# Performance work log

Hardware: AMD Instinct MI355X
Metric: run time of the kernel (lower is better)

Reference implementation:

```python
import jax, jax.numpy as jnp
import numpy as np

V, N, K, D = 100000, 20000, 32, 128
NEG = -1e9  # masked logit value


def setup_inputs() -> dict:
    key = jax.random.key(0)
    ks = jax.random.split(key, 8)
    return {
        "nodes": jax.random.randint(ks[0], (N,), 0, V),
        "neigh_idx": jax.random.randint(ks[1], (N, K), 0, V),
        "degrees": jax.random.randint(ks[2], (N,), 0, K + 1),
        "u2e": jax.random.normal(ks[3], (V, D), dtype=jnp.float32),
        "W1": jax.random.normal(ks[4], (2 * D, D), dtype=jnp.float32) * 0.05,
        "b1": jnp.zeros((D,), jnp.float32),
        "W2": jax.random.normal(ks[5], (D, D), dtype=jnp.float32) * 0.05,
        "b2": jnp.zeros((D,), jnp.float32),
        "W3": jax.random.normal(ks[6], (D, 1), dtype=jnp.float32) * 0.05,
        "b3": jnp.zeros((1,), jnp.float32),
    }


def reference(nodes, neigh_idx, degrees, u2e, W1, b1, W2, b2, W3, b3):
    self_feats = u2e[nodes]                      # [N, D]
    e_u = u2e[neigh_idx]                         # [N, K, D] ragged gather (padded)
    # Attention MLP: cat(neighbor, self) -> relu -> relu -> scalar logit
    x = jnp.concatenate([e_u, jnp.broadcast_to(self_feats[:, None, :], (e_u.shape[0], K, D))], axis=-1)  # [N, K, 2D]
    h = jax.nn.relu(x @ W1 + b1)                 # [N, K, D]
    h = jax.nn.relu(h @ W2 + b2)                 # [N, K, D]
    logits = (h @ W3 + b3)[..., 0]               # [N, K]
    mask = jnp.arange(K)[None, :] < degrees[:, None]
    att = jax.nn.softmax(jnp.where(mask, logits, NEG), axis=-1)  # softmax over neighbors
    agg = jnp.einsum("nk,nkd->nd", att, e_u)     # attention-weighted neighbor sum
    out = jnp.where(degrees[:, None] > 0, (agg + self_feats) * 0.5, self_feats)
    return out
```

## Files before the change

### kernel.cpp

```cpp
#include <hip/hip_runtime.h>
#include <hip/hip_bf16.h>

#define KK 32
#define DD 128
#define NEGV (-1e9f)
#define SE 136

typedef __attribute__((ext_vector_type(8))) short bf16x8;
typedef __attribute__((ext_vector_type(4))) float f32x4;

__device__ __forceinline__ unsigned short f2bf(float f) {
    union { float f; unsigned u; } v; v.f = f;
    unsigned r = v.u + 0x7fffu + ((v.u >> 16) & 1u);
    return (unsigned short)(r >> 16);
}
__device__ __forceinline__ float bf2f(unsigned short h) {
    union { unsigned u; float f; } v; v.u = ((unsigned)h) << 16;
    return v.f;
}
__device__ __forceinline__ unsigned pk2(float x, float y) {
    union { __hip_bfloat162 h; unsigned u; } c;
    c.h = __float22bfloat162_rn(float2{x, y});
    return c.u;
}

__global__ __launch_bounds__(256) void prep_kernel(
    const float* __restrict__ u2e, const float* __restrict__ W1, const float* __restrict__ W2,
    unsigned short* __restrict__ u2e_bf, unsigned short* __restrict__ W1t,
    unsigned short* __restrict__ W2t, const int u2e_blocks)
{
    const int b = blockIdx.x;
    if (b < u2e_blocks) {
        const long base = (long)b * 4096 + threadIdx.x * 16;
        const float4* s = (const float4*)(u2e + base);
        const float4 v0 = s[0], v1 = s[1], v2 = s[2], v3 = s[3];
        uint4 p0, p1;
        p0.x = pk2(v0.x, v0.y); p0.y = pk2(v0.z, v0.w);
        p0.z = pk2(v1.x, v1.y); p0.w = pk2(v1.z, v1.w);
        p1.x = pk2(v2.x, v2.y); p1.y = pk2(v2.z, v2.w);
        p1.z = pk2(v3.x, v3.y); p1.w = pk2(v3.z, v3.w);
        *(uint4*)(u2e_bf + base)     = p0;
        *(uint4*)(u2e_bf + base + 8) = p1;
    } else {
        const int id = (b - u2e_blocks) * 256 + threadIdx.x;
        if (id < 256 * 128) {
            const int n = id >> 8, k = id & 255;
            W1t[id] = f2bf(W1[k * DD + n]);
        } else {
            const int j = id - 256 * 128;
            const int n = j >> 7, k = j & 127;
            W2t[j] = f2bf(W2[k * DD + n]);
        }
    }
}

template<bool BF>
__global__ __launch_bounds__(256, 2) void ppagg_mfma(
    const int* __restrict__ nodes, const int* __restrict__ neigh,
    const int* __restrict__ degrees, const float* __restrict__ u2e,
    const unsigned short* __restrict__ u2e_bf,
    const unsigned short* __restrict__ W1t, const unsigned short* __restrict__ W2t,
    const float* __restrict__ b1, const float* __restrict__ b2,
    const float* __restrict__ W3, const float* __restrict__ b3,
    float* __restrict__ out, const int Nn)
{
    __shared__ __align__(16) unsigned short s_A[128 * SE];
    __shared__ __align__(16) unsigned short s_B[128 * SE];
    __shared__ __align__(16) unsigned short s_x[4 * DD];
    __shared__ float s_part[4][128];
    __shared__ float s_att[128];

    const int tid  = threadIdx.x;
    const int w    = tid >> 6;
    const int lane = tid & 63;
    const int ln   = lane & 15;
    const int q    = lane >> 4;

    const int nb = blockIdx.x * 8;
    const int r  = tid & 127;
    const int h  = tid >> 7;

    int idxA, idxB, vA, vB;
    {
        int ng0 = nb + (r >> 5);       if (ng0 >= Nn) ng0 = Nn - 1;
        int ng1 = nb + 4 + (r >> 5);   if (ng1 >= Nn) ng1 = Nn - 1;
        idxA = neigh[ng0 * KK + (r & 31)];
        idxB = neigh[ng1 * KK + (r & 31)];
        vA = (r & 31) < degrees[ng0];
        vB = (r & 31) < degrees[ng1];
    }
    float2 self0, self1;
    {
        int n0 = nb + w;       if (n0 >= Nn) n0 = Nn - 1;
        int n1 = nb + 4 + w;   if (n1 >= Nn) n1 = Nn - 1;
        self0 = *(const float2*)(u2e + (long)nodes[n0] * DD + lane * 2);
        self1 = *(const float2*)(u2e + (long)nodes[n1] * DD + lane * 2);
    }

    auto stage = [&](unsigned short* buf, int idx, int v) {
        unsigned short* dst = buf + r * SE + h * 64;
        if (BF && v) {
            const uint4* src = (const uint4*)(u2e_bf + (long)idx * DD + h * 64);
            #pragma unroll
            for (int c = 0; c < 8; ++c) *(uint4*)(dst + c * 8) = src[c];
        } else if (!BF && v) {
            const float4* src = (const float4*)(u2e + (long)idx * DD + h * 64);
            #pragma unroll
            for (int c8 = 0; c8 < 8; ++c8) {
                const float4 v0 = src[c8 * 2];
                const float4 v1 = src[c8 * 2 + 1];
                uint4 p;
                p.x = pk2(v0.x, v0.y); p.y = pk2(v0.z, v0.w);
                p.z = pk2(v1.x, v1.y); p.w = pk2(v1.z, v1.w);
                *(uint4*)(dst + c8 * 8) = p;
            }
        } else {
            const uint4 z = {0u, 0u, 0u, 0u};
            #pragma unroll
            for (int c = 0; c < 8; ++c) *(uint4*)(dst + c * 8) = z;
        }
    };

    stage(s_A, idxA, vA);
    *(unsigned*)(s_x + w * DD + lane * 2) = pk2(self0.x, self0.y);

    bf16x8 b1f[8][2], b2f[4][2];
    float b1c[2], b2c[2], w3c[2];
    const int c0 = w * 32 + ln;
    const int c1 = c0 + 16;
    #pragma unroll
    for (int kk = 0; kk < 8; ++kk) {
        b1f[kk][0] = *(const bf16x8*)(W1t + c0 * 256 + kk * 32 + q * 8);
        b1f[kk][1] = *(const bf16x8*)(W1t + c1 * 256 + kk * 32 + q * 8);
    }
    #pragma unroll
    for (int kk = 0; kk < 4; ++kk) {
        b2f[kk][0] = *(const bf16x8*)(W2t + c0 * 128 + kk * 32 + q * 8);
        b2f[kk][1] = *(const bf16x8*)(W2t + c1 * 128 + kk * 32 + q * 8);
    }
    b1c[0] = b1[c0]; b1c[1] = b1[c1];
    b2c[0] = b2[c0]; b2c[1] = b2[c1];
    w3c[0] = W3[c0]; w3c[1] = W3[c1];
    const float b3v = b3[0];

    __syncthreads();

    #pragma unroll
    for (int it = 0; it < 2; ++it) {
        unsigned short* E = it ? s_B : s_A;
        unsigned short* H = it ? s_A : s_B;
        const int gbase = nb + it * 4;
        const float2 selfv = it ? self1 : self0;

        if (it == 1) __syncthreads();

        f32x4 acc[8][2];
        #pragma unroll
        for (int mt = 0; mt < 8; ++mt) {
            acc[mt][0] = (f32x4){0.f, 0.f, 0.f, 0.f};
            acc[mt][1] = (f32x4){0.f, 0.f, 0.f, 0.f};
        }
        #pragma unroll
        for (int kk = 0; kk < 4; ++kk) {
            bf16x8 a[8];
            #pragma unroll
            for (int mt = 0; mt < 8; ++mt)
                a[mt] = *(const bf16x8*)(E + (mt * 16 + ln) * SE + kk * 32 + q * 8);
            #pragma unroll
            for (int mt = 0; mt < 8; ++mt) {
                acc[mt][0] = __builtin_amdgcn_mfma_f32_16x16x32_bf16(a[mt], b1f[kk][0], acc[mt][0], 0, 0, 0);
                acc[mt][1] = __builtin_amdgcn_mfma_f32_16x16x32_bf16(a[mt], b1f[kk][1], acc[mt][1], 0, 0, 0);
            }
        }
        #pragma unroll
        for (int kk = 4; kk < 8; ++kk) {
            #pragma unroll
            for (int mt = 0; mt < 8; ++mt) {
                const bf16x8 a = *(const bf16x8*)(s_x + (mt >> 1) * DD + (kk - 4) * 32 + q * 8);
                acc[mt][0] = __builtin_amdgcn_mfma_f32_16x16x32_bf16(a, b1f[kk][0], acc[mt][0], 0, 0, 0);
                acc[mt][1] = __builtin_amdgcn_mfma_f32_16x16x32_bf16(a, b1f[kk][1], acc[mt][1], 0, 0, 0);
            }
        }
        #pragma unroll
        for (int mt = 0; mt < 8; ++mt)
            #pragma unroll
            for (int nt = 0; nt < 2; ++nt) {
                const int c = nt ? c1 : c0;
                #pragma unroll
                for (int rr = 0; rr < 4; rr += 2) {
                    const unsigned p = pk2(fmaxf(acc[mt][nt][rr]     + b1c[nt], 0.f),
                                           fmaxf(acc[mt][nt][rr + 1] + b1c[nt], 0.f));
                    const int row = mt * 16 + q * 4 + rr;
                    H[row * SE + c]       = (unsigned short)(p & 0xffffu);
                    H[(row + 1) * SE + c] = (unsigned short)(p >> 16);
                }
            }
        __syncthreads();

        f32x4 acc2[8][2];
        #pragma unroll
        for (int mt = 0; mt < 8; ++mt) {
            acc2[mt][0] = (f32x4){0.f, 0.f, 0.f, 0.f};
            acc2[mt][1] = (f32x4){0.f, 0.f, 0.f, 0.f};
        }
        #pragma unroll
        for (int kk = 0; kk < 4; ++kk) {
            bf16x8 a[8];
            #pragma unroll
            for (int mt = 0; mt < 8; ++mt)
                a[mt] = *(const bf16x8*)(H + (mt * 16 + ln) * SE + kk * 32 + q * 8);
            #pragma unroll
            for (int mt = 0; mt < 8; ++mt) {
                acc2[mt][0] = __builtin_amdgcn_mfma_f32_16x16x32_bf16(a[mt], b2f[kk][0], acc2[mt][0], 0, 0, 0);
                acc2[mt][1] = __builtin_amdgcn_mfma_f32_16x16x32_bf16(a[mt], b2f[kk][1], acc2[mt][1], 0, 0, 0);
            }
        }
        #pragma unroll
        for (int mt = 0; mt < 8; ++mt) {
            float p[4];
            #pragma unroll
            for (int rr = 0; rr < 4; ++rr) {
                const float h0 = fmaxf(acc2[mt][0][rr] + b2c[0], 0.f);
                const float h1v = fmaxf(acc2[mt][1][rr] + b2c[1], 0.f);
                p[rr] = fmaf(h0, w3c[0], h1v * w3c[1]);
            }
            #pragma unroll
            for (int off = 1; off < 16; off <<= 1) {
                #pragma unroll
                for (int rr = 0; rr < 4; ++rr) p[rr] += __shfl_xor(p[rr], off);
            }
            if (ln == 0) {
                const int row0 = mt * 16 + q * 4;
                #pragma unroll
                for (int rr = 0; rr < 4; ++rr) s_part[w][row0 + rr] = p[rr];
            }
        }
        __syncthreads();

        if (it == 0) {
            stage(s_B, idxB, vB);
            *(unsigned*)(s_x + w * DD + lane * 2) = pk2(self1.x, self1.y);
        }

        if (tid < 128) {
            const int row = tid;
            const float logit = s_part[0][row] + s_part[1][row] + s_part[2][row] + s_part[3][row] + b3v;
            int ng = gbase + (row >> 5);
            if (ng >= Nn) ng = Nn - 1;
            const int deg = degrees[ng];
            const float ml = ((row & 31) < deg) ? logit : NEGV;
            float mx = ml;
            #pragma unroll
            for (int off = 16; off > 0; off >>= 1) mx = fmaxf(mx, __shfl_xor(mx, off));
            const float e = __expf(ml - mx);
            float ssum = e;
            #pragma unroll
            for (int off = 16; off > 0; off >>= 1) ssum += __shfl_xor(ssum, off);
            s_att[row] = e / ssum;
        }
        __syncthreads();

        {
            const int ng = gbase + w;
            const int degw = (ng < Nn) ? degrees[ng] : 0;
            float ax = 0.f, ay = 0.f;
            for (int k = 0; k < degw; ++k) {
                const float a = s_att[w * KK + k];
                const unsigned pe = *(const unsigned*)(E + (w * KK + k) * SE + lane * 2);
                ax = fmaf(a, bf2f((unsigned short)(pe & 0xffffu)), ax);
                ay = fmaf(a, bf2f((unsigned short)(pe >> 16)), ay);
            }
            if (ng < Nn) {
                float2 o;
                o.x = (degw > 0) ? 0.5f * (ax + selfv.x) : selfv.x;
                o.y = (degw > 0) ? 0.5f * (ay + selfv.y) : selfv.y;
                *(float2*)(out + (long)ng * DD + lane * 2) = o;
            }
        }
    }
}

extern "C" void kernel_launch(void* const* d_in, const int* in_sizes, int n_in,
                              void* d_out, int out_size, void* d_ws, size_t ws_size,
                              hipStream_t stream) {
    const int*   nodes   = (const int*)d_in[0];
    const int*   neigh   = (const int*)d_in[1];
    const int*   degrees = (const int*)d_in[2];
    const float* u2e     = (const float*)d_in[3];
    const float* W1      = (const float*)d_in[4];
    const float* b1      = (const float*)d_in[5];
    const float* W2      = (const float*)d_in[6];
    const float* b2      = (const float*)d_in[7];
    const float* W3      = (const float*)d_in[8];
    const float* b3      = (const float*)d_in[9];
    float* out = (float*)d_out;

    const int  Nn = in_sizes[0];
    const long Vd = (long)in_sizes[3];

    unsigned short* W1t = (unsigned short*)d_ws;
    unsigned short* W2t = W1t + 256 * 128;
    unsigned short* u2e_bf = W2t + 128 * 128;

    const size_t need_bf = (size_t)(256 * 128 + 128 * 128) * 2 + (size_t)Vd * 2;
    const bool use_bf = (ws_size >= need_bf) && (Vd % 4096 == 0);
    const int u2e_blocks = use_bf ? (int)(Vd / 4096) : 0;

    prep_kernel<<<u2e_blocks + 192, 256, 0, stream>>>(u2e, W1, W2, u2e_bf, W1t, W2t, u2e_blocks);

    const int grid = (Nn + 7) / 8;
    if (use_bf)
        ppagg_mfma<true><<<grid, 256, 0, stream>>>(nodes, neigh, degrees, u2e, u2e_bf,
                                                   W1t, W2t, b1, b2, W3, b3, out, Nn);
    else
        ppagg_mfma<false><<<grid, 256, 0, stream>>>(nodes, neigh, degrees, u2e, nullptr,
                                                    W1t, W2t, b1, b2, W3, b3, out, Nn);
}
```

Baseline: 222.4 us.

## Split MLP columns across eight waves with 512-thread blocks

Doubles the block to 512 threads (8 waves) so each wave computes 16 output columns instead of 32 in both MLP layers, halving per-wave accumulator and weight-fragment registers. Staging, self-feature loads and the weighted aggregation are redistributed over the larger thread count, and the logit reduction now sums eight partials. This aims to raise occupancy and latency hiding. In exchange, each A-fragment load from LDS feeds half as many MFMAs, and the 512-thread blocks with roughly 72KB of shared memory may limit how many blocks fit per CU.

Measured after the change: 253.0 us. +13.8%, slower.

```diff
diff --git a/kernel.cpp b/kernel.cpp
--- a/kernel.cpp
+++ b/kernel.cpp
@@ -55,7 +55,7 @@
 }
 
 template<bool BF>
-__global__ __launch_bounds__(256, 2) void ppagg_mfma(
+__global__ __launch_bounds__(512, 4) void ppagg_mfma(
     const int* __restrict__ nodes, const int* __restrict__ neigh,
     const int* __restrict__ degrees, const float* __restrict__ u2e,
     const unsigned short* __restrict__ u2e_bf,
@@ -66,8 +66,8 @@
 {
     __shared__ __align__(16) unsigned short s_A[128 * SE];
     __shared__ __align__(16) unsigned short s_B[128 * SE];
-    __shared__ __align__(16) unsigned short s_x[4 * DD];
-    __shared__ float s_part[4][128];
+    __shared__ __align__(16) unsigned short s_x8[8 * DD];
+    __shared__ float s_part[8][128];
     __shared__ float s_att[128];
 
     const int tid  = threadIdx.x;
@@ -77,8 +77,10 @@
     const int q    = lane >> 4;
 
     const int nb = blockIdx.x * 8;
-    const int r  = tid & 127;
-    const int h  = tid >> 7;
+    const int c  = w * 16 + ln;
+
+    const int r  = tid >> 2;
+    const int qt = tid & 3;
 
     int idxA, idxB, vA, vB;
     {
@@ -89,24 +91,17 @@
         vA = (r & 31) < degrees[ng0];
         vB = (r & 31) < degrees[ng1];
     }
-    float2 self0, self1;
-    {
-        int n0 = nb + w;       if (n0 >= Nn) n0 = Nn - 1;
-        int n1 = nb + 4 + w;   if (n1 >= Nn) n1 = Nn - 1;
-        self0 = *(const float2*)(u2e + (long)nodes[n0] * DD + lane * 2);
-        self1 = *(const float2*)(u2e + (long)nodes[n1] * DD + lane * 2);
-    }
 
     auto stage = [&](unsigned short* buf, int idx, int v) {
-        unsigned short* dst = buf + r * SE + h * 64;
+        unsigned short* dst = buf + r * SE + qt * 32;
         if (BF && v) {
-            const uint4* src = (const uint4*)(u2e_bf + (long)idx * DD + h * 64);
-            #pragma unroll
-            for (int c = 0; c < 8; ++c) *(uint4*)(dst + c * 8) = src[c];
+            const uint4* src = (const uint4*)(u2e_bf + (long)idx * DD + qt * 32);
+            #pragma unroll
+            for (int cc = 0; cc < 4; ++cc) *(uint4*)(dst + cc * 8) = src[cc];
         } else if (!BF && v) {
-            const float4* src = (const float4*)(u2e + (long)idx * DD + h * 64);
-            #pragma unroll
-            for (int c8 = 0; c8 < 8; ++c8) {
+            const float4* src = (const float4*)(u2e + (long)idx * DD + qt * 32);
+            #pragma unroll
+            for (int c8 = 0; c8 < 4; ++c8) {
                 const float4 v0 = src[c8 * 2];
                 const float4 v1 = src[c8 * 2 + 1];
                 uint4 p;
@@ -117,30 +112,32 @@
         } else {
             const uint4 z = {0u, 0u, 0u, 0u};
             #pragma unroll
-            for (int c = 0; c < 8; ++c) *(uint4*)(dst + c * 8) = z;
+            for (int cc = 0; cc < 4; ++cc) *(uint4*)(dst + cc * 8) = z;
         }
     };
 
     stage(s_A, idxA, vA);
-    *(unsigned*)(s_x + w * DD + lane * 2) = pk2(self0.x, self0.y);
-
-    bf16x8 b1f[8][2], b2f[4][2];
-    float b1c[2], b2c[2], w3c[2];
-    const int c0 = w * 32 + ln;
-    const int c1 = c0 + 16;
-    #pragma unroll
-    for (int kk = 0; kk < 8; ++kk) {
-        b1f[kk][0] = *(const bf16x8*)(W1t + c0 * 256 + kk * 32 + q * 8);
-        b1f[kk][1] = *(const bf16x8*)(W1t + c1 * 256 + kk * 32 + q * 8);
-    }
-    #pragma unroll
-    for (int kk = 0; kk < 4; ++kk) {
-        b2f[kk][0] = *(const bf16x8*)(W2t + c0 * 128 + kk * 32 + q * 8);
-        b2f[kk][1] = *(const bf16x8*)(W2t + c1 * 128 + kk * 32 + q * 8);
-    }
-    b1c[0] = b1[c0]; b1c[1] = b1[c1];
-    b2c[0] = b2[c0]; b2c[1] = b2[c1];
-    w3c[0] = W3[c0]; w3c[1] = W3[c1];
+
+    {
+        int n = nb + w; if (n >= Nn) n = Nn - 1;
+        const float2 sv = *(const float2*)(u2e + (long)nodes[n] * DD + lane * 2);
+        *(unsigned*)(s_x8 + w * DD + lane * 2) = pk2(sv.x, sv.y);
+    }
+    float selfs[2];
+    #pragma unroll
+    for (int t = 0; t < 2; ++t) {
+        int gn = nb + t * 4 + (w >> 1); if (gn >= Nn) gn = Nn - 1;
+        selfs[t] = u2e[(long)nodes[gn] * DD + (w & 1) * 64 + lane];
+    }
+
+    bf16x8 b1f[8], b2f[4];
+    #pragma unroll
+    for (int kk = 0; kk < 8; ++kk)
+        b1f[kk] = *(const bf16x8*)(W1t + c * 256 + kk * 32 + q * 8);
+    #pragma unroll
+    for (int kk = 0; kk < 4; ++kk)
+        b2f[kk] = *(const bf16x8*)(W2t + c * 128 + kk * 32 + q * 8);
+    const float b1c = b1[c], b2c = b2[c], w3c = W3[c];
     const float b3v = b3[0];
 
     __syncthreads();
@@ -150,80 +147,58 @@
         unsigned short* E = it ? s_B : s_A;
         unsigned short* H = it ? s_A : s_B;
         const int gbase = nb + it * 4;
-        const float2 selfv = it ? self1 : self0;
 
         if (it == 1) __syncthreads();
 
-        f32x4 acc[8][2];
+        f32x4 acc[8];
+        #pragma unroll
+        for (int mt = 0; mt < 8; ++mt) acc[mt] = (f32x4){0.f, 0.f, 0.f, 0.f};
+        #pragma unroll
+        for (int kk = 0; kk < 4; ++kk) {
+            #pragma unroll
+            for (int mt = 0; mt < 8; ++mt) {
+                const bf16x8 a = *(const bf16x8*)(E + (mt * 16 + ln) * SE + kk * 32 + q * 8);
+                acc[mt] = __builtin_amdgcn_mfma_f32_16x16x32_bf16(a, b1f[kk], acc[mt], 0, 0, 0);
+            }
+        }
+        #pragma unroll
+        for (int kk = 4; kk < 8; ++kk) {
+            #pragma unroll
+            for (int mt = 0; mt < 8; ++mt) {
+                const bf16x8 a = *(const bf16x8*)(s_x8 + (it * 4 + (mt >> 1)) * DD + (kk - 4) * 32 + q * 8);
+                acc[mt] = __builtin_amdgcn_mfma_f32_16x16x32_bf16(a, b1f[kk], acc[mt], 0, 0, 0);
+            }
+        }
         #pragma unroll
         for (int mt = 0; mt < 8; ++mt) {
-            acc[mt][0] = (f32x4){0.f, 0.f, 0.f, 0.f};
-            acc[mt][1] = (f32x4){0.f, 0.f, 0.f, 0.f};
-        }
+            #pragma unroll
+            for (int rr = 0; rr < 4; rr += 2) {
+                const unsigned p = pk2(fmaxf(acc[mt][rr]     + b1c, 0.f),
+                                       fmaxf(acc[mt][rr + 1] + b1c, 0.f));
+                const int row = mt * 16 + q * 4 + rr;
+                H[row * SE + c]       = (unsigned short)(p & 0xffffu);
+                H[(row + 1) * SE + c] = (unsigned short)(p >> 16);
+            }
+        }
+        __syncthreads();
+
+        f32x4 acc2[8];
+        #pragma unroll
+        for (int mt = 0; mt < 8; ++mt) acc2[mt] = (f32x4){0.f, 0.f, 0.f, 0.f};
         #pragma unroll
         for (int kk = 0; kk < 4; ++kk) {
-            bf16x8 a[8];
-            #pragma unroll
-            for (int mt = 0; mt < 8; ++mt)
-                a[mt] = *(const bf16x8*)(E + (mt * 16 + ln) * SE + kk * 32 + q * 8);
             #pragma unroll
             for (int mt = 0; mt < 8; ++mt) {
-                acc[mt][0] = __builtin_amdgcn_mfma_f32_16x16x32_bf16(a[mt], b1f[kk][0], acc[mt][0], 0, 0, 0);
-                acc[mt][1] = __builtin_amdgcn_mfma_f32_16x16x32_bf16(a[mt], b1f[kk][1], acc[mt][1], 0, 0, 0);
-            }
-        }
-        #pragma unroll
-        for (int kk = 4; kk < 8; ++kk) {
-            #pragma unroll
-            for (int mt = 0; mt < 8; ++mt) {
-                const bf16x8 a = *(const bf16x8*)(s_x + (mt >> 1) * DD + (kk - 4) * 32 + q * 8);
-                acc[mt][0] = __builtin_amdgcn_mfma_f32_16x16x32_bf16(a, b1f[kk][0], acc[mt][0], 0, 0, 0);
-                acc[mt][1] = __builtin_amdgcn_mfma_f32_16x16x32_bf16(a, b1f[kk][1], acc[mt][1], 0, 0, 0);
-            }
-        }
-        #pragma unroll
-        for (int mt = 0; mt < 8; ++mt)
-            #pragma unroll
-            for (int nt = 0; nt < 2; ++nt) {
-                const int c = nt ? c1 : c0;
-                #pragma unroll
-                for (int rr = 0; rr < 4; rr += 2) {
-                    const unsigned p = pk2(fmaxf(acc[mt][nt][rr]     + b1c[nt], 0.f),
-                                           fmaxf(acc[mt][nt][rr + 1] + b1c[nt], 0.f));
-                    const int row = mt * 16 + q * 4 + rr;
-                    H[row * SE + c]       = (unsigned short)(p & 0xffffu);
-                    H[(row + 1) * SE + c] = (unsigned short)(p >> 16);
-                }
-            }
-        __syncthreads();
-
-        f32x4 acc2[8][2];
-        #pragma unroll
-        for (int mt = 0; mt < 8; ++mt) {
-            acc2[mt][0] = (f32x4){0.f, 0.f, 0.f, 0.f};
-            acc2[mt][1] = (f32x4){0.f, 0.f, 0.f, 0.f};
-        }
-        #pragma unroll
-        for (int kk = 0; kk < 4; ++kk) {
-            bf16x8 a[8];
-            #pragma unroll
-            for (int mt = 0; mt < 8; ++mt)
-                a[mt] = *(const bf16x8*)(H + (mt * 16 + ln) * SE + kk * 32 + q * 8);
-            #pragma unroll
-            for (int mt = 0; mt < 8; ++mt) {
-                acc2[mt][0] = __builtin_amdgcn_mfma_f32_16x16x32_bf16(a[mt], b2f[kk][0], acc2[mt][0], 0, 0, 0);
-                acc2[mt][1] = __builtin_amdgcn_mfma_f32_16x16x32_bf16(a[mt], b2f[kk][1], acc2[mt][1], 0, 0, 0);
+                const bf16x8 a = *(const bf16x8*)(H + (mt * 16 + ln) * SE + kk * 32 + q * 8);
+                acc2[mt] = __builtin_amdgcn_mfma_f32_16x16x32_bf16(a, b2f[kk], acc2[mt], 0, 0, 0);
             }
         }
         #pragma unroll
         for (int mt = 0; mt < 8; ++mt) {
             float p[4];
             #pragma unroll
-            for (int rr = 0; rr < 4; ++rr) {
-                const float h0 = fmaxf(acc2[mt][0][rr] + b2c[0], 0.f);
-                const float h1v = fmaxf(acc2[mt][1][rr] + b2c[1], 0.f);
-                p[rr] = fmaf(h0, w3c[0], h1v * w3c[1]);
-            }
+            for (int rr = 0; rr < 4; ++rr)
+                p[rr] = fmaxf(acc2[mt][rr] + b2c, 0.f) * w3c;
             #pragma unroll
             for (int off = 1; off < 16; off <<= 1) {
                 #pragma unroll
@@ -237,14 +212,13 @@
         }
         __syncthreads();
 
-        if (it == 0) {
-            stage(s_B, idxB, vB);
-            *(unsigned*)(s_x + w * DD + lane * 2) = pk2(self1.x, self1.y);
-        }
+        if (it == 0) stage(s_B, idxB, vB);
 
         if (tid < 128) {
             const int row = tid;
-            const float logit = s_part[0][row] + s_part[1][row] + s_part[2][row] + s_part[3][row] + b3v;
+            float logit = b3v;
+            #pragma unroll
+            for (int ww = 0; ww < 8; ++ww) logit += s_part[ww][row];
             int ng = gbase + (row >> 5);
             if (ng >= Nn) ng = Nn - 1;
             const int deg = degrees[ng];
@@ -261,20 +235,18 @@
         __syncthreads();
 
         {
-            const int ng = gbase + w;
+            const int nd = w >> 1;
+            const int ng = gbase + nd;
             const int degw = (ng < Nn) ? degrees[ng] : 0;
-            float ax = 0.f, ay = 0.f;
+            const int col = (w & 1) * 64 + lane;
+            float ax = 0.f;
             for (int k = 0; k < degw; ++k) {
-                const float a = s_att[w * KK + k];
-                const unsigned pe = *(const unsigned*)(E + (w * KK + k) * SE + lane * 2);
-                ax = fmaf(a, bf2f((unsigned short)(pe & 0xffffu)), ax);
-                ay = fmaf(a, bf2f((unsigned short)(pe >> 16)), ay);
+                const float a = s_att[nd * KK + k];
+                ax = fmaf(a, bf2f(E[(nd * KK + k) * SE + col]), ax);
             }
             if (ng < Nn) {
-                float2 o;
-                o.x = (degw > 0) ? 0.5f * (ax + selfv.x) : selfv.x;
-                o.y = (degw > 0) ? 0.5f * (ay + selfv.y) : selfv.y;
-                *(float2*)(out + (long)ng * DD + lane * 2) = o;
+                const float sv = selfs[it];
+                out[(long)ng * DD + col] = (degw > 0) ? 0.5f * (ax + sv) : sv;
             }
         }
     }
@@ -310,9 +282,9 @@
 
     const int grid = (Nn + 7) / 8;
     if (use_bf)
-        ppagg_mfma<true><<<grid, 256, 0, stream>>>(nodes, neigh, degrees, u2e, u2e_bf,
+        ppagg_mfma<true><<<grid, 512, 0, stream>>>(nodes, neigh, degrees, u2e, u2e_bf,
                                                    W1t, W2t, b1, b2, W3, b3, out, Nn);
     else
-        ppagg_mfma<false><<<grid, 256, 0, stream>>>(nodes, neigh, degrees, u2e, nullptr,
+        ppagg_mfma<false><<<grid, 512, 0, stream>>>(nodes, neigh, degrees, u2e, nullptr,
                                                     W1t, W2t, b1, b2, W3, b3, out, Nn);
 }
```

## Precompute self-feature half of first layer once per node instead of per neighbor

Applied to the files above, without the earlier changes.

The self-feature half of the first MLP layer (self @ W1[D:]) is identical for all 32 neighbors of a node, but was computed redundantly in every neighbor row tile. The change computes it once per block for all 8 nodes with a small MFMA pass, stores the biased result in shared memory, and adds it during the ReLU epilogue. This halves the layer-1 MFMA work and the W1 register fragments, at the cost of an extra shared buffer, an extra barrier and a small prologue GEMM that is mostly idle (8 of 16 rows used).

Result: no change. 221.8 us (-0.3%).

```diff
diff --git a/kernel.cpp b/kernel.cpp
--- a/kernel.cpp
+++ b/kernel.cpp
@@ -66,7 +66,8 @@
 {
     __shared__ __align__(16) unsigned short s_A[128 * SE];
     __shared__ __align__(16) unsigned short s_B[128 * SE];
-    __shared__ __align__(16) unsigned short s_x[4 * DD];
+    __shared__ __align__(16) unsigned short s_x8[8 * DD];
+    __shared__ float s_selfc[8 * 128];
     __shared__ float s_part[4][128];
     __shared__ float s_att[128];
 
@@ -89,13 +90,6 @@
         vA = (r & 31) < degrees[ng0];
         vB = (r & 31) < degrees[ng1];
     }
-    float2 self0, self1;
-    {
-        int n0 = nb + w;       if (n0 >= Nn) n0 = Nn - 1;
-        int n1 = nb + 4 + w;   if (n1 >= Nn) n1 = Nn - 1;
-        self0 = *(const float2*)(u2e + (long)nodes[n0] * DD + lane * 2);
-        self1 = *(const float2*)(u2e + (long)nodes[n1] * DD + lane * 2);
-    }
 
     auto stage = [&](unsigned short* buf, int idx, int v) {
         unsigned short* dst = buf + r * SE + h * 64;
@@ -122,19 +116,31 @@
     };
 
     stage(s_A, idxA, vA);
-    *(unsigned*)(s_x + w * DD + lane * 2) = pk2(self0.x, self0.y);
-
-    bf16x8 b1f[8][2], b2f[4][2];
+
+    {
+        int gn = nb + (tid >> 5); if (gn >= Nn) gn = Nn - 1;
+        const int g = tid >> 5, p = tid & 31;
+        const float4 v = *(const float4*)(u2e + (long)nodes[gn] * DD + p * 4);
+        *(unsigned*)(s_x8 + g * DD + p * 4)     = pk2(v.x, v.y);
+        *(unsigned*)(s_x8 + g * DD + p * 4 + 2) = pk2(v.z, v.w);
+    }
+
+    float2 self0, self1;
+    {
+        int n0 = nb + w;       if (n0 >= Nn) n0 = Nn - 1;
+        int n1 = nb + 4 + w;   if (n1 >= Nn) n1 = Nn - 1;
+        self0 = *(const float2*)(u2e + (long)nodes[n0] * DD + lane * 2);
+        self1 = *(const float2*)(u2e + (long)nodes[n1] * DD + lane * 2);
+    }
+
+    bf16x8 b1f[4][2], b2f[4][2];
     float b1c[2], b2c[2], w3c[2];
     const int c0 = w * 32 + ln;
     const int c1 = c0 + 16;
     #pragma unroll
-    for (int kk = 0; kk < 8; ++kk) {
+    for (int kk = 0; kk < 4; ++kk) {
         b1f[kk][0] = *(const bf16x8*)(W1t + c0 * 256 + kk * 32 + q * 8);
         b1f[kk][1] = *(const bf16x8*)(W1t + c1 * 256 + kk * 32 + q * 8);
-    }
-    #pragma unroll
-    for (int kk = 0; kk < 4; ++kk) {
         b2f[kk][0] = *(const bf16x8*)(W2t + c0 * 128 + kk * 32 + q * 8);
         b2f[kk][1] = *(const bf16x8*)(W2t + c1 * 128 + kk * 32 + q * 8);
     }
@@ -143,6 +149,26 @@
     w3c[0] = W3[c0]; w3c[1] = W3[c1];
     const float b3v = b3[0];
 
+    __syncthreads();
+
+    {
+        f32x4 a0 = (f32x4){0.f,0.f,0.f,0.f}, a1 = (f32x4){0.f,0.f,0.f,0.f};
+        #pragma unroll
+        for (int kk = 0; kk < 4; ++kk) {
+            const bf16x8 av = *(const bf16x8*)(s_x8 + (ln & 7) * DD + kk * 32 + q * 8);
+            const bf16x8 w0 = *(const bf16x8*)(W1t + c0 * 256 + 128 + kk * 32 + q * 8);
+            const bf16x8 w1 = *(const bf16x8*)(W1t + c1 * 256 + 128 + kk * 32 + q * 8);
+            a0 = __builtin_amdgcn_mfma_f32_16x16x32_bf16(av, w0, a0, 0, 0, 0);
+            a1 = __builtin_amdgcn_mfma_f32_16x16x32_bf16(av, w1, a1, 0, 0, 0);
+        }
+        if (q < 2) {
+            #pragma unroll
+            for (int rr = 0; rr < 4; ++rr) {
+                s_selfc[(q * 4 + rr) * 128 + c0] = a0[rr] + b1c[0];
+                s_selfc[(q * 4 + rr) * 128 + c1] = a1[rr] + b1c[1];
+            }
+        }
+    }
     __syncthreads();
 
     #pragma unroll
@@ -173,28 +199,22 @@
             }
         }
         #pragma unroll
-        for (int kk = 4; kk < 8; ++kk) {
-            #pragma unroll
-            for (int mt = 0; mt < 8; ++mt) {
-                const bf16x8 a = *(const bf16x8*)(s_x + (mt >> 1) * DD + (kk - 4) * 32 + q * 8);
-                acc[mt][0] = __builtin_amdgcn_mfma_f32_16x16x32_bf16(a, b1f[kk][0], acc[mt][0], 0, 0, 0);
-                acc[mt][1] = __builtin_amdgcn_mfma_f32_16x16x32_bf16(a, b1f[kk][1], acc[mt][1], 0, 0, 0);
-            }
-        }
-        #pragma unroll
-        for (int mt = 0; mt < 8; ++mt)
-            #pragma unroll
-            for (int nt = 0; nt < 2; ++nt) {
-                const int c = nt ? c1 : c0;
-                #pragma unroll
-                for (int rr = 0; rr < 4; rr += 2) {
-                    const unsigned p = pk2(fmaxf(acc[mt][nt][rr]     + b1c[nt], 0.f),
-                                           fmaxf(acc[mt][nt][rr + 1] + b1c[nt], 0.f));
-                    const int row = mt * 16 + q * 4 + rr;
-                    H[row * SE + c]       = (unsigned short)(p & 0xffffu);
-                    H[(row + 1) * SE + c] = (unsigned short)(p >> 16);
-                }
-            }
+        for (int mt = 0; mt < 8; ++mt) {
+            const float sc0 = s_selfc[(it * 4 + (mt >> 1)) * 128 + c0];
+            const float sc1 = s_selfc[(it * 4 + (mt >> 1)) * 128 + c1];
+            #pragma unroll
+            for (int rr = 0; rr < 4; rr += 2) {
+                const int row = mt * 16 + q * 4 + rr;
+                const unsigned p0 = pk2(fmaxf(acc[mt][0][rr]     + sc0, 0.f),
+                                        fmaxf(acc[mt][0][rr + 1] + sc0, 0.f));
+                const unsigned p1v = pk2(fmaxf(acc[mt][1][rr]     + sc1, 0.f),
+                                         fmaxf(acc[mt][1][rr + 1] + sc1, 0.f));
+                H[row * SE + c0]       = (unsigned short)(p0 & 0xffffu);
+                H[(row + 1) * SE + c0] = (unsigned short)(p0 >> 16);
+                H[row * SE + c1]       = (unsigned short)(p1v & 0xffffu);
+                H[(row + 1) * SE + c1] = (unsigned short)(p1v >> 16);
+            }
+        }
         __syncthreads();
 
         f32x4 acc2[8][2];
@@ -237,10 +257,7 @@
         }
         __syncthreads();
 
-        if (it == 0) {
-            stage(s_B, idxB, vB);
-            *(unsigned*)(s_x + w * DD + lane * 2) = pk2(self1.x, self1.y);
-        }
+        if (it == 0) stage(s_B, idxB, vB);
 
         if (tid < 128) {
             const int row = tid;
```
